# Optimization experiments

Hardware: AMD Instinct MI355X
Metric: run time of the kernel (lower is better)

## Reference

```python
import jax, jax.numpy as jnp
import numpy as np

C_IN, H, T_OUT, C_OUT = 16, 256, 24, 8


def setup_inputs() -> dict:
    key = jax.random.key(0)
    ks = jax.random.split(key, 8)
    s_ih = 1.0 / np.sqrt(H)
    x = jax.random.normal(ks[0], (8192, C_IN, 48), dtype=jnp.float32)
    # Encoder LSTMCell params (PyTorch layout: gates stacked [i, f, g, o], each H rows)
    enc_Wih = jax.random.uniform(ks[1], (4 * H, C_IN), minval=-s_ih, maxval=s_ih, dtype=jnp.float32)
    enc_Whh = jax.random.uniform(ks[2], (4 * H, H), minval=-s_ih, maxval=s_ih, dtype=jnp.float32)
    enc_b = jax.random.uniform(ks[3], (4 * H,), minval=-s_ih, maxval=s_ih, dtype=jnp.float32)  # b_ih + b_hh folded
    # Decoder LSTMCell has input_size=0 -> W_ih is (4H, 0), contributes nothing
    dec_Whh = jax.random.uniform(ks[4], (4 * H, H), minval=-s_ih, maxval=s_ih, dtype=jnp.float32)
    dec_b = jax.random.uniform(ks[5], (4 * H,), minval=-s_ih, maxval=s_ih, dtype=jnp.float32)
    # TimestepDense: per-timestep (non-shared) linear H -> C_OUT, dropout inactive at eval
    dense_W = jax.random.uniform(ks[6], (T_OUT, C_OUT, H), minval=-s_ih, maxval=s_ih, dtype=jnp.float32)
    dense_b = jax.random.uniform(ks[7], (T_OUT, C_OUT), minval=-s_ih, maxval=s_ih, dtype=jnp.float32)
    return {"x": x, "enc_Wih": enc_Wih, "enc_Whh": enc_Whh, "enc_b": enc_b,
            "dec_Whh": dec_Whh, "dec_b": dec_b, "dense_W": dense_W, "dense_b": dense_b}


def _lstm_step(h, c, gates):
    i, f, g, o = jnp.split(gates, 4, axis=-1)
    c_new = jax.nn.sigmoid(f) * c + jax.nn.sigmoid(i) * jnp.tanh(g)
    h_new = jax.nn.sigmoid(o) * jnp.tanh(c_new)
    return h_new, c_new


def reference(x, enc_Wih, enc_Whh, enc_b, dec_Whh, dec_b, dense_W, dense_b):
    N = x.shape[0]
    # ----- Encoder: scan over T input steps -----
    xt = jnp.transpose(x, (2, 0, 1))  # (T, N, C)
    h0 = jnp.zeros((N, H), dtype=x.dtype)
    c0 = jnp.zeros((N, H), dtype=x.dtype)

    def enc_step(carry, x_t):
        h, c = carry
        gates = x_t @ enc_Wih.T + h @ enc_Whh.T + enc_b  # (N, 4H)
        h, c = _lstm_step(h, c, gates)
        return (h, c), None

    (h_enc, _), _ = jax.lax.scan(enc_step, (h0, c0), xt)

    # ----- Decoder: zero-input LSTM cell, collect hidden states -----
    def dec_step(carry, _):
        h, c = carry
        gates = h @ dec_Whh.T + dec_b
        h, c = _lstm_step(h, c, gates)
        return (h, c), h

    (_, _), hs = jax.lax.scan(dec_step, (h_enc, c0), None, length=T_OUT)  # hs: (T_OUT, N, H)

    # ----- TimestepDense: per-timestep linear H -> C_OUT (eval mode, dropout off) -----
    out = jnp.einsum('tnh,toh->not', hs, dense_W) + dense_b.T[None]  # (N, C_OUT, T_OUT)
    return out
```

## Files before the change

kernel.cpp:

```cpp
#include <hip/hip_runtime.h>

typedef __attribute__((ext_vector_type(8))) _Float16 f16x8;
typedef __attribute__((ext_vector_type(4))) float    f32x4;

#define HD    256
#define CIN   16
#define TIN   48
#define TOUT  24
#define COUT  8
#define MB    32
#define KPAD  296
#define KT_ENC 9
#define KT_DEC 8
#define WE_HALVES (KT_ENC*4*16*512)
#define WD_HALVES (KT_DEC*4*16*512)
#define PREP_TOTAL (WE_HALVES + WD_HALVES)

template <int N> struct KTag { static constexpr int val = N; };

__global__ void prep_frags(const float* __restrict__ enc_Wih,
                           const float* __restrict__ enc_Whh,
                           const float* __restrict__ dec_Whh,
                           _Float16* __restrict__ wf)
{
    int p = blockIdx.x * blockDim.x + threadIdx.x;
    if (p >= PREP_TOTAL) return;
    int lane = (p >> 3) & 63;
    int s    = p & 7;
    int kq   = ((lane >> 4) << 3) + s;
    int l15  = lane & 15;
    float v;
    if (p < WE_HALVES) {
        int frag = p >> 9;
        int kt = frag >> 6, g = (frag >> 4) & 3, ntile = frag & 15;
        int k   = kt * 32 + kq;
        int row = g * 256 + ntile * 16 + l15;
        v = 0.0f;
        if (k < 256)      v = enc_Whh[row * 256 + k];
        else if (k < 272) v = enc_Wih[row * 16 + (k - 256)];
    } else {
        int q = p - WE_HALVES;
        int frag = q >> 9;
        int kt = frag >> 6, g = (frag >> 4) & 3, ntile = frag & 15;
        int k   = kt * 32 + kq;
        int row = g * 256 + ntile * 16 + l15;
        v = dec_Whh[row * 256 + k];
    }
    wf[p] = (_Float16)v;
}

__device__ __forceinline__ float sigm(float v) {
    return __builtin_amdgcn_rcpf(1.0f + __expf(-v));
}
__device__ __forceinline__ float tanh_f(float v) {
    return 1.0f - 2.0f * __builtin_amdgcn_rcpf(1.0f + __expf(2.0f * v));
}

__global__ __launch_bounds__(1024, 1) void seq2seq_mfma(
    const float* __restrict__ x,
    const _Float16* __restrict__ wf,
    const float* __restrict__ enc_b,
    const float* __restrict__ dec_b,
    const float* __restrict__ denseW,
    const float* __restrict__ denseb,
    float* __restrict__ out)
{
    __shared__ __align__(16) _Float16 hF[MB * KPAD];
    __shared__ __align__(16) _Float16 xs[2][MB * CIN * 8];
    __shared__ __align__(16) float    outS[MB * COUT * TOUT];

    const int tid  = threadIdx.x;
    const int w    = tid >> 6;
    const int lane = tid & 63;
    const int quad = lane >> 4;
    const int l15  = lane & 15;
    const int n0   = blockIdx.x * MB;

    float bE[4], bD[4];
    #pragma unroll
    for (int g = 0; g < 4; ++g) {
        int col = w * 16 + l15;
        bE[g] = enc_b[g * 256 + col];
        bD[g] = dec_b[g * 256 + col];
    }

    auto loadchunk = [&](int wd) {
        if (tid < 512) {
            int m = tid >> 4, c = tid & 15;
            const float* xp = x + (size_t)(n0 + m) * (CIN * TIN) + c * TIN + wd * 8;
            float4 v0 = *(const float4*)xp;
            float4 v1 = *(const float4*)(xp + 4);
            f16x8 hv = { (_Float16)v0.x, (_Float16)v0.y, (_Float16)v0.z, (_Float16)v0.w,
                         (_Float16)v1.x, (_Float16)v1.y, (_Float16)v1.z, (_Float16)v1.w };
            *(f16x8*)(&xs[wd & 1][m * (CIN * 8) + c * 8]) = hv;
        }
    };
    auto xcopy = [&](int t) {
        if (tid < 512) {
            int m = tid >> 4, c = tid & 15;
            hF[m * KPAD + 256 + c] = xs[(t >> 3) & 1][m * (CIN * 8) + c * 8 + (t & 7)];
        }
    };

    for (int i = tid; i < MB * KPAD; i += 1024) hF[i] = (_Float16)0.0f;
    loadchunk(0);
    __syncthreads();
    xcopy(0);
    __syncthreads();

    f32x4 acc[2][4];
    float cst[2][4];
    #pragma unroll
    for (int mt = 0; mt < 2; ++mt)
        #pragma unroll
        for (int r = 0; r < 4; ++r) cst[mt][r] = 0.0f;

    const f16x8* Ap0 = (const f16x8*)(hF + l15 * KPAD);
    const f16x8* Ap1 = (const f16x8*)(hF + (16 + l15) * KPAD);
    const f16x8* WpE = (const f16x8*)wf + w * 64 + lane;
    const f16x8* WpD = (const f16x8*)(wf + WE_HALVES) + w * 64 + lane;

    auto gemm = [&](auto kt_tag, const f16x8* __restrict__ Wp, const float (&bias)[4]) {
        constexpr int KT = decltype(kt_tag)::val;
        #pragma unroll
        for (int mt = 0; mt < 2; ++mt)
            #pragma unroll
            for (int g = 0; g < 4; ++g) {
                float b = bias[g];
                f32x4 bv = {b, b, b, b};
                acc[mt][g] = bv;
            }
        #pragma unroll
        for (int kt = 0; kt < KT; ++kt) {
            f16x8 a0 = Ap0[kt * 4 + quad];
            f16x8 a1 = Ap1[kt * 4 + quad];
            #pragma unroll
            for (int g = 0; g < 4; ++g) {
                f16x8 bf = Wp[(kt * 4 + g) * 1024];
                acc[0][g] = __builtin_amdgcn_mfma_f32_16x16x32_f16(a0, bf, acc[0][g], 0, 0, 0);
                acc[1][g] = __builtin_amdgcn_mfma_f32_16x16x32_f16(a1, bf, acc[1][g], 0, 0, 0);
            }
        }
    };

    auto pointwise = [&]() {
        int col = w * 16 + l15;
        #pragma unroll
        for (int mt = 0; mt < 2; ++mt)
            #pragma unroll
            for (int r = 0; r < 4; ++r) {
                float iv = sigm(acc[mt][0][r]);
                float fv = sigm(acc[mt][1][r]);
                float gv = tanh_f(acc[mt][2][r]);
                float ov = sigm(acc[mt][3][r]);
                float cn = fmaf(fv, cst[mt][r], iv * gv);
                cst[mt][r] = cn;
                float hv = ov * tanh_f(cn);
                hF[(mt * 16 + quad * 4 + r) * KPAD + col] = (_Float16)hv;
            }
    };

    for (int t = 0; t < TIN; ++t) {
        gemm(KTag<KT_ENC>{}, WpE, bE);
        __syncthreads();
        pointwise();
        if ((t & 7) == 0 && (t >> 3) + 1 < 6) loadchunk((t >> 3) + 1);
        if (t + 1 < TIN) xcopy(t + 1);
        __syncthreads();
    }

    #pragma unroll
    for (int mt = 0; mt < 2; ++mt)
        #pragma unroll
        for (int r = 0; r < 4; ++r) cst[mt][r] = 0.0f;

    for (int t = 0; t < TOUT; ++t) {
        gemm(KTag<KT_DEC>{}, WpD, bD);
        __syncthreads();
        pointwise();
        __syncthreads();
        if (tid < MB * COUT) {
            int m = tid >> 3, o = tid & 7;
            const float* wr = denseW + (t * COUT + o) * HD;
            float s = denseb[t * COUT + o];
            #pragma unroll 4
            for (int j8 = 0; j8 < 32; ++j8) {
                f16x8 hv  = *(const f16x8*)(hF + m * KPAD + j8 * 8);
                float4 w0 = *(const float4*)(wr + j8 * 8);
                float4 w1 = *(const float4*)(wr + j8 * 8 + 4);
                s = fmaf((float)hv[0], w0.x, s);
                s = fmaf((float)hv[1], w0.y, s);
                s = fmaf((float)hv[2], w0.z, s);
                s = fmaf((float)hv[3], w0.w, s);
                s = fmaf((float)hv[4], w1.x, s);
                s = fmaf((float)hv[5], w1.y, s);
                s = fmaf((float)hv[6], w1.z, s);
                s = fmaf((float)hv[7], w1.w, s);
            }
            outS[m * (COUT * TOUT) + o * TOUT + t] = s;
        }
    }

    __syncthreads();
    {
        const float4* src = (const float4*)outS;
        float4* dst = (float4*)(out + (size_t)n0 * (COUT * TOUT));
        for (int i = tid; i < MB * COUT * TOUT / 4; i += 1024)
            dst[i] = src[i];
    }
}

extern "C" void kernel_launch(void* const* d_in, const int* in_sizes, int n_in,
                              void* d_out, int out_size, void* d_ws, size_t ws_size,
                              hipStream_t stream) {
    const float* x       = (const float*)d_in[0];
    const float* enc_Wih = (const float*)d_in[1];
    const float* enc_Whh = (const float*)d_in[2];
    const float* enc_b   = (const float*)d_in[3];
    const float* dec_Whh = (const float*)d_in[4];
    const float* dec_b   = (const float*)d_in[5];
    const float* denseW  = (const float*)d_in[6];
    const float* denseb  = (const float*)d_in[7];
    float* out = (float*)d_out;
    _Float16* wf = (_Float16*)d_ws;

    prep_frags<<<(PREP_TOTAL + 255) / 256, 256, 0, stream>>>(enc_Wih, enc_Whh, dec_Whh, wf);
    seq2seq_mfma<<<8192 / MB, 1024, 0, stream>>>(x, wf, enc_b, dec_b, denseW, denseb, out);
}
```

Baseline: 1.406 ms.

## Stream LSTM weight fragments into LDS with double-buffered async global_load_lds

Per-step weight fragments are now loaded with global_load_lds into a per-wave double buffer in LDS, prefetching the next k-tile while MFMAs run on the current one, instead of direct global vector loads. The x input is no longer staged in 8-step chunks; each step loads the next timestep's scalar before the GEMM and writes it after pointwise. Output is flushed every 4 decoder steps via a small LDS buffer rather than a full staging array at the end. The intent is to hide weight-load latency; the cost is extra LDS and tight vmcnt waits that may serialize.

```diff
diff --git a/kernel.cpp b/kernel.cpp
--- a/kernel.cpp
+++ b/kernel.cpp
@@ -56,6 +56,12 @@
     return 1.0f - 2.0f * __builtin_amdgcn_rcpf(1.0f + __expf(2.0f * v));
 }
 
+__device__ __forceinline__ void gld_lds16(const _Float16* g, _Float16* l) {
+    __builtin_amdgcn_global_load_lds(
+        (const __attribute__((address_space(1))) void*)g,
+        (__attribute__((address_space(3))) void*)l, 16, 0, 0);
+}
+
 __global__ __launch_bounds__(1024, 1) void seq2seq_mfma(
     const float* __restrict__ x,
     const _Float16* __restrict__ wf,
@@ -66,8 +72,8 @@
     float* __restrict__ out)
 {
     __shared__ __align__(16) _Float16 hF[MB * KPAD];
-    __shared__ __align__(16) _Float16 xs[2][MB * CIN * 8];
-    __shared__ __align__(16) float    outS[MB * COUT * TOUT];
+    __shared__ __align__(16) _Float16 Wlds[16][2][4][512];
+    __shared__ __align__(16) float    outS4[MB * COUT * 4];
 
     const int tid  = threadIdx.x;
     const int w    = tid >> 6;
@@ -84,28 +90,12 @@
         bD[g] = dec_b[g * 256 + col];
     }
 
-    auto loadchunk = [&](int wd) {
-        if (tid < 512) {
-            int m = tid >> 4, c = tid & 15;
-            const float* xp = x + (size_t)(n0 + m) * (CIN * TIN) + c * TIN + wd * 8;
-            float4 v0 = *(const float4*)xp;
-            float4 v1 = *(const float4*)(xp + 4);
-            f16x8 hv = { (_Float16)v0.x, (_Float16)v0.y, (_Float16)v0.z, (_Float16)v0.w,
-                         (_Float16)v1.x, (_Float16)v1.y, (_Float16)v1.z, (_Float16)v1.w };
-            *(f16x8*)(&xs[wd & 1][m * (CIN * 8) + c * 8]) = hv;
-        }
-    };
-    auto xcopy = [&](int t) {
-        if (tid < 512) {
-            int m = tid >> 4, c = tid & 15;
-            hF[m * KPAD + 256 + c] = xs[(t >> 3) & 1][m * (CIN * 8) + c * 8 + (t & 7)];
-        }
-    };
-
     for (int i = tid; i < MB * KPAD; i += 1024) hF[i] = (_Float16)0.0f;
-    loadchunk(0);
     __syncthreads();
-    xcopy(0);
+    if (tid < 512) {
+        int m = tid >> 4, c = tid & 15;
+        hF[m * KPAD + 256 + c] = (_Float16)x[(size_t)(n0 + m) * (CIN * TIN) + c * TIN];
+    }
     __syncthreads();
 
     f32x4 acc[2][4];
@@ -117,10 +107,16 @@
 
     const f16x8* Ap0 = (const f16x8*)(hF + l15 * KPAD);
     const f16x8* Ap1 = (const f16x8*)(hF + (16 + l15) * KPAD);
-    const f16x8* WpE = (const f16x8*)wf + w * 64 + lane;
-    const f16x8* WpD = (const f16x8*)(wf + WE_HALVES) + w * 64 + lane;
-
-    auto gemm = [&](auto kt_tag, const f16x8* __restrict__ Wp, const float (&bias)[4]) {
+
+    auto stage = [&](int buf, int kt, const _Float16* __restrict__ Wbase) {
+        #pragma unroll
+        for (int g = 0; g < 4; ++g) {
+            const _Float16* gp = Wbase + (size_t)(kt * 64 + g * 16 + w) * 512 + lane * 8;
+            gld_lds16(gp, &Wlds[w][buf][g][0]);
+        }
+    };
+
+    auto gemm = [&](auto kt_tag, const _Float16* __restrict__ Wbase, const float (&bias)[4]) {
         constexpr int KT = decltype(kt_tag)::val;
         #pragma unroll
         for (int mt = 0; mt < 2; ++mt)
@@ -130,13 +126,22 @@
                 f32x4 bv = {b, b, b, b};
                 acc[mt][g] = bv;
             }
+        stage(0, 0, Wbase);
         #pragma unroll
         for (int kt = 0; kt < KT; ++kt) {
+            if (kt + 1 < KT) {
+                stage((kt + 1) & 1, kt + 1, Wbase);
+                asm volatile("s_waitcnt vmcnt(4)" ::: "memory");
+            } else {
+                asm volatile("s_waitcnt vmcnt(0)" ::: "memory");
+            }
+            __builtin_amdgcn_sched_barrier(0);
             f16x8 a0 = Ap0[kt * 4 + quad];
             f16x8 a1 = Ap1[kt * 4 + quad];
+            const int b = kt & 1;
             #pragma unroll
             for (int g = 0; g < 4; ++g) {
-                f16x8 bf = Wp[(kt * 4 + g) * 1024];
+                f16x8 bf = *(const f16x8*)&Wlds[w][b][g][lane * 8];
                 acc[0][g] = __builtin_amdgcn_mfma_f32_16x16x32_f16(a0, bf, acc[0][g], 0, 0, 0);
                 acc[1][g] = __builtin_amdgcn_mfma_f32_16x16x32_f16(a1, bf, acc[1][g], 0, 0, 0);
             }
@@ -161,11 +166,14 @@
     };
 
     for (int t = 0; t < TIN; ++t) {
-        gemm(KTag<KT_ENC>{}, WpE, bE);
+        float xv = 0.0f;
+        const bool xl = (tid < 512) && (t + 1 < TIN);
+        if (xl)
+            xv = x[(size_t)(n0 + (tid >> 4)) * (CIN * TIN) + (tid & 15) * TIN + (t + 1)];
+        gemm(KTag<KT_ENC>{}, wf, bE);
         __syncthreads();
         pointwise();
-        if ((t & 7) == 0 && (t >> 3) + 1 < 6) loadchunk((t >> 3) + 1);
-        if (t + 1 < TIN) xcopy(t + 1);
+        if (xl) hF[(tid >> 4) * KPAD + 256 + (tid & 15)] = (_Float16)xv;
         __syncthreads();
     }
 
@@ -175,7 +183,7 @@
         for (int r = 0; r < 4; ++r) cst[mt][r] = 0.0f;
 
     for (int t = 0; t < TOUT; ++t) {
-        gemm(KTag<KT_DEC>{}, WpD, bD);
+        gemm(KTag<KT_DEC>{}, wf + WE_HALVES, bD);
         __syncthreads();
         pointwise();
         __syncthreads();
@@ -197,16 +205,12 @@
                 s = fmaf((float)hv[6], w1.z, s);
                 s = fmaf((float)hv[7], w1.w, s);
             }
-            outS[m * (COUT * TOUT) + o * TOUT + t] = s;
+            outS4[(tid << 2) | (t & 3)] = s;
+            if ((t & 3) == 3) {
+                float4 v = *(const float4*)&outS4[tid << 2];
+                *(float4*)(out + (size_t)(n0 + m) * (COUT * TOUT) + o * TOUT + (t - 3)) = v;
+            }
         }
-    }
-
-    __syncthreads();
-    {
-        const float4* src = (const float4*)outS;
-        float4* dst = (float4*)(out + (size_t)n0 * (COUT * TOUT));
-        for (int i = tid; i < MB * COUT * TOUT / 4; i += 1024)
-            dst[i] = src[i];
     }
 }
 
```

After: 1.139 ms. -19.0%, faster.
